# Optimization experiments

Hardware: AMD Instinct MI355X
Metric: run time of the kernel (lower is better)

Reference implementation:

```python
import jax, jax.numpy as jnp
import numpy as np

DIM = 1024
NUM_HEADS = 16
HEAD_DIM = DIM // NUM_HEADS
SCALE = HEAD_DIM ** (-0.5)


def setup_inputs() -> dict:
    key = jax.random.key(0)
    ks = jax.random.split(key, 10)
    b, nq, nkv = 1, 4096, 4096
    s = DIM ** -0.5
    return {
        "q": jax.random.normal(ks[0], (b, nq, DIM), jnp.float32),
        "kv": jax.random.normal(ks[1], (b, nkv, DIM), jnp.float32),
        "q_w": jax.random.normal(ks[2], (DIM, DIM), jnp.float32) * s,
        "q_b": jnp.zeros((DIM,), jnp.float32),
        "k_w": jax.random.normal(ks[3], (DIM, DIM), jnp.float32) * s,
        "k_b": jnp.zeros((DIM,), jnp.float32),
        "v_w": jax.random.normal(ks[4], (DIM, DIM), jnp.float32) * s,
        "v_b": jnp.zeros((DIM,), jnp.float32),
        "o_w": jax.random.normal(ks[5], (DIM, DIM), jnp.float32) * s,
        "o_b": jnp.zeros((DIM,), jnp.float32),
    }


def reference(q, kv, q_w, q_b, k_w, k_b, v_w, v_b, o_w, o_b):
    b, nq, _ = q.shape
    nkv = kv.shape[1]
    h, c = NUM_HEADS, HEAD_DIM
    # projections (torch Linear: x @ W^T + b); split into heads
    qh = (q @ q_w.T + q_b).reshape(b, nq, h, c).transpose(0, 2, 1, 3)   # b h nq c
    kh = (kv @ k_w.T + k_b).reshape(b, nkv, h, c).transpose(0, 2, 1, 3)  # b h nkv c
    vh = (kv @ v_w.T + v_b).reshape(b, nkv, h, c).transpose(0, 2, 1, 3)  # b h nkv c
    # full attention score matrix (non-fused, as in source)
    attn = jnp.einsum('bhqc,bhkc->bhqk', qh, kh) * SCALE
    attn = jax.nn.softmax(attn, axis=-1)
    out = jnp.einsum('bhqk,bhkc->bhqc', attn, vh)  # b h nq c
    out = out.transpose(0, 2, 1, 3).reshape(b, nq, h * c)
    out = out @ o_w.T + o_b
    return out
```

## Files before the change

kernel.cpp:

```cpp
#include <hip/hip_runtime.h>


typedef unsigned short ushort_t;
typedef unsigned short ushort4v __attribute__((ext_vector_type(4)));
typedef unsigned short ushort8 __attribute__((ext_vector_type(8)));
typedef __bf16 bf16x8 __attribute__((ext_vector_type(8)));
typedef float f32x4 __attribute__((ext_vector_type(4)));
typedef float f32x16 __attribute__((ext_vector_type(16)));
typedef unsigned int uint4v __attribute__((ext_vector_type(4)));

#define SEQ 4096
#define DIM 1024
#define NH 16
#define HD 64
#define QSCALE 0.18033688011112042f

__device__ inline ushort_t fcvt(float f) {
    return __builtin_bit_cast(ushort_t, (__bf16)f);
}
__device__ inline bf16x8 frag_of(ushort8 t) {
    return __builtin_bit_cast(bf16x8, t);
}
__device__ inline bf16x8 lds_frag(const ushort_t* p) {
    return frag_of(*(const ushort8*)p);
}
__device__ inline unsigned pk2(float a, float b) {
    return (unsigned)fcvt(a) | ((unsigned)fcvt(b) << 16);
}
__device__ inline void plswap(unsigned& a, unsigned& b) {
    asm("v_permlane32_swap_b32 %0, %1" : "+v"(a), "+v"(b));
}
__device__ inline int swz(int row, int col) {
    return row * 64 + (col ^ ((row & 7) << 3));
}
__device__ inline int xcd_swz(int bid, int nwg) {
    return (bid & 7) * (nwg >> 3) + (bid >> 3);
}
__device__ __attribute__((always_inline)) inline void gload16(
    const ushort_t* g, ushort_t* l)
{
    __builtin_amdgcn_global_load_lds(
        (const __attribute__((address_space(1))) void*)g,
        (__attribute__((address_space(3))) void*)l, 16, 0, 0);
}

__global__ __launch_bounds__(256) void cvt2(
    const float* __restrict__ s0, ushort_t* __restrict__ d0,
    const float* __restrict__ s1, ushort_t* __restrict__ d1, int n8)
{
    const float* s = blockIdx.y ? s1 : s0;
    ushort_t*    d = blockIdx.y ? d1 : d0;
    int i = blockIdx.x * 256 + threadIdx.x;
    if (i >= n8) return;
    const f32x4* sp = (const f32x4*)s + (size_t)i * 2;
    f32x4 a = sp[0], b = sp[1];
    ushort8 o;
    for (int k = 0; k < 4; ++k) { o[k] = fcvt(a[k]); o[k + 4] = fcvt(b[k]); }
    *((ushort8*)d + i) = o;
}

__global__ __launch_bounds__(256) void cvt4(
    const float* __restrict__ s0, ushort_t* __restrict__ d0,
    const float* __restrict__ s1, ushort_t* __restrict__ d1,
    const float* __restrict__ s2, ushort_t* __restrict__ d2,
    const float* __restrict__ s3, ushort_t* __restrict__ d3, int n8)
{
    const float* ss[4] = {s0, s1, s2, s3};
    ushort_t*    dd[4] = {d0, d1, d2, d3};
    const float* s = ss[blockIdx.y];
    ushort_t*    d = dd[blockIdx.y];
    int i = blockIdx.x * 256 + threadIdx.x;
    if (i >= n8) return;
    const f32x4* sp = (const f32x4*)s + (size_t)i * 2;
    f32x4 a = sp[0], b = sp[1];
    ushort8 o;
    for (int k = 0; k < 4; ++k) { o[k] = fcvt(a[k]); o[k + 4] = fcvt(b[k]); }
    *((ushort8*)d + i) = o;
}

template<int BM, int BN>
__device__ __attribute__((always_inline)) inline void gemm_core3(
    const ushort_t* __restrict__ A, const ushort_t* __restrict__ W,
    int m0, int n0, int tid, f32x4 (&acc)[BM / 32][BN / 32], ushort_t* sLDS)
{
    constexpr int TA = BM * 32;
    constexpr int TB = BN * 32;
    ushort_t* const aB0 = sLDS;
    ushort_t* const aB1 = sLDS + TA;
    ushort_t* const bB0 = sLDS + 2 * TA;
    ushort_t* const bB1 = sLDS + 2 * TA + TB;

    const int w    = tid >> 6;
    const int lane = tid & 63;
    const int quad = lane >> 4;
    const int l15  = lane & 15;
    const int wm   = w >> 1;
    const int wn   = w & 1;

    const int srow = lane >> 2;
    const int sch  = (((lane & 3) ^ ((lane >> 3) & 3)) << 3);
    const ushort_t* Ag = A + (size_t)(m0 + w * (BM / 4) + srow) * DIM + sch;
    const ushort_t* Bg = W + (size_t)(n0 + w * (BN / 4) + srow) * DIM + sch;
    const int aOff = w * (BM / 4) * 32;
    const int bOff = w * (BN / 4) * 32;

    for (int i = 0; i < BM / 64; ++i)
        gload16(Ag + (size_t)(i * 16) * DIM, aB0 + aOff + i * 512);
    for (int i = 0; i < BN / 64; ++i)
        gload16(Bg + (size_t)(i * 16) * DIM, bB0 + bOff + i * 512);
    __syncthreads();

    const int slot = (quad ^ ((l15 >> 1) & 3)) << 3;
    for (int it = 0; it < DIM / 32; ++it) {
        const int cur = it & 1;
        ushort_t* aC = cur ? aB1 : aB0;
        ushort_t* bC = cur ? bB1 : bB0;
        ushort_t* aN = cur ? aB0 : aB1;
        ushort_t* bN = cur ? bB0 : bB1;

        if (it + 1 < DIM / 32) {
            const int k0 = (it + 1) * 32;
            for (int i = 0; i < BM / 64; ++i)
                gload16(Ag + k0 + (size_t)(i * 16) * DIM, aN + aOff + i * 512);
            for (int i = 0; i < BN / 64; ++i)
                gload16(Bg + k0 + (size_t)(i * 16) * DIM, bN + bOff + i * 512);
        }

        bf16x8 af[BM / 32], bf[BN / 32];
        for (int i = 0; i < BM / 32; ++i) {
            int row = wm * (BM / 2) + i * 16 + l15;
            af[i] = lds_frag(aC + row * 32 + slot);
        }
        for (int j = 0; j < BN / 32; ++j) {
            int row = wn * (BN / 2) + j * 16 + l15;
            bf[j] = lds_frag(bC + row * 32 + slot);
        }
        for (int i = 0; i < BM / 32; ++i)
            for (int j = 0; j < BN / 32; ++j)
                acc[i][j] = __builtin_amdgcn_mfma_f32_16x16x32_bf16(
                    af[i], bf[j], acc[i][j], 0, 0, 0);
        __syncthreads();
    }
}

__global__ __launch_bounds__(256, 3) void proj3(
    const ushort_t* __restrict__ Qb, const ushort_t* __restrict__ KVb,
    const ushort_t* __restrict__ qwb, const ushort_t* __restrict__ kwb,
    const ushort_t* __restrict__ vwb,
    const float* __restrict__ q_b, const float* __restrict__ k_b,
    const float* __restrict__ v_b,
    ushort_t* __restrict__ Qp, ushort_t* __restrict__ Kp,
    ushort_t* __restrict__ VpT)
{
    __shared__ __align__(1024) ushort_t sLDS[17536];

    const int lb = xcd_swz(blockIdx.x, 768);
    const int z  = lb >> 8;
    const int r  = lb & 255;
    const int m0 = (r >> 3) * 128;
    const int n0 = (r & 7) * 128;

    const ushort_t* A = z ? KVb : Qb;
    const ushort_t* W = (z == 0) ? qwb : (z == 1 ? kwb : vwb);
    const float* bias = (z == 0) ? q_b : (z == 1 ? k_b : v_b);
    const int tid = threadIdx.x;

    f32x4 acc[4][4] = {};
    gemm_core3<128, 128>(A, W, m0, n0, tid, acc, sLDS);

    const int lane = tid & 63, quad = lane >> 4, l15 = lane & 15;
    const int wm = (tid >> 6) >> 1, wn = (tid >> 6) & 1;

    if (z == 2) {
        const int TSTR = 136;
        for (int j = 0; j < 4; ++j) {
            int col = wn * 64 + j * 16 + l15;
            float bj = bias[n0 + col];
            for (int i = 0; i < 4; ++i) {
                int row = wm * 64 + i * 16 + quad * 4;
                ushort4v o4;
                for (int r2 = 0; r2 < 4; ++r2) o4[r2] = fcvt(acc[i][j][r2] + bj);
                *(ushort4v*)(sLDS + col * TSTR + row) = o4;
            }
        }
        __syncthreads();
        const int vrow = tid >> 1;
        const int vc   = (tid & 1) * 64;
        ushort_t* dst = VpT + (size_t)(n0 + vrow) * SEQ + m0 + vc;
        const ushort_t* src = sLDS + vrow * TSTR + vc;
        for (int k = 0; k < 8; ++k)
            *(ushort8*)(dst + k * 8) = *(const ushort8*)(src + k * 8);
    } else {
        const float scale = (z == 0) ? QSCALE : 1.0f;
        ushort_t* C = z ? Kp : Qp;
        for (int j = 0; j < 4; ++j) {
            int col = n0 + wn * 64 + j * 16 + l15;
            float bj = bias[col];
            for (int i = 0; i < 4; ++i) {
                int row = m0 + wm * 64 + i * 16 + quad * 4;
                for (int r2 = 0; r2 < 4; ++r2)
                    C[(size_t)(row + r2) * DIM + col] =
                        fcvt((acc[i][j][r2] + bj) * scale);
            }
        }
    }
}

__global__ __launch_bounds__(256, 4) void gemm_out(
    const ushort_t* __restrict__ A, const ushort_t* __restrict__ W,
    const float* __restrict__ bias, float* __restrict__ C)
{
    __shared__ __align__(1024) ushort_t sLDS[8192];

    const int lb = xcd_swz(blockIdx.x, 1024);
    const int m0 = (lb >> 4) * 64;
    const int n0 = (lb & 15) * 64;
    const int tid = threadIdx.x;

    f32x4 acc[2][2] = {};
    gemm_core3<64, 64>(A, W, m0, n0, tid, acc, sLDS);

    const int lane = tid & 63, quad = lane >> 4, l15 = lane & 15;
    const int wm = (tid >> 6) >> 1, wn = (tid >> 6) & 1;
    for (int j = 0; j < 2; ++j) {
        int col = n0 + wn * 32 + j * 16 + l15;
        float bj = bias[col];
        for (int i = 0; i < 2; ++i) {
            int row = m0 + wm * 32 + i * 16 + quad * 4;
            for (int r = 0; r < 4; ++r)
                C[(size_t)(row + r) * DIM + col] = acc[i][j][r] + bj;
        }
    }
}

#define TILE 4096
#define BUFE (2 * TILE)
__global__ __launch_bounds__(256, 2) void attn_kernel(
    const ushort_t* __restrict__ Q, const ushort_t* __restrict__ K,
    const ushort_t* __restrict__ VT, ushort_t* __restrict__ O)
{
    __shared__ __align__(16) ushort_t sB[2 * BUFE];

    const int lb   = xcd_swz(blockIdx.x, 512);
    const int h    = lb >> 5;
    const int qblk = lb & 31;

    const int tid  = threadIdx.x;
    const int w    = tid >> 6;
    const int lane = tid & 63;
    const int l31  = lane & 31;
    const int hi   = lane >> 5;
    const int q0   = qblk * 128 + w * 32;
    const int hHD  = h * HD;

    const int srow0 = tid >> 3;
    const int srow1 = srow0 + 32;
    const int sch   = (tid & 7) << 3;
    const ushort_t* Kg0 = K  + (size_t)srow0 * DIM + hHD + sch;
    const ushort_t* Kg1 = K  + (size_t)srow1 * DIM + hHD + sch;
    const ushort_t* Vg0 = VT + (size_t)(hHD + srow0) * SEQ + sch;
    const ushort_t* Vg1 = VT + (size_t)(hHD + srow1) * SEQ + sch;
    const int lk0 = swz(srow0, sch), lk1 = swz(srow1, sch);

    const ushort_t* qb = Q + (size_t)(q0 + l31) * DIM + hHD + hi * 8;
    bf16x8 qf[4];
    for (int ks = 0; ks < 4; ++ks)
        qf[ks] = frag_of(*(const ushort8*)(qb + ks * 16));

    *(ushort8*)(sB + lk0)        = *(const ushort8*)(Kg0);
    *(ushort8*)(sB + lk1)        = *(const ushort8*)(Kg1);
    *(ushort8*)(sB + TILE + lk0) = *(const ushort8*)(Vg0);
    *(ushort8*)(sB + TILE + lk1) = *(const ushort8*)(Vg1);
    __syncthreads();

    f32x16 oacc[2] = {};
    float l_i = 0.f;

    for (int it = 0; it < SEQ / 64; ++it) {
        const int cur = it & 1;
        const int kvn = (it + 1) * 64;
        ushort_t* bK = sB + cur * BUFE;
        ushort_t* bV = bK + TILE;

        ushort8 gk0, gk1, gv0, gv1;
        if (kvn < SEQ) {
            gk0 = *(const ushort8*)(Kg0 + (size_t)kvn * DIM);
            gk1 = *(const ushort8*)(Kg1 + (size_t)kvn * DIM);
            gv0 = *(const ushort8*)(Vg0 + kvn);
            gv1 = *(const ushort8*)(Vg1 + kvn);
        }

        bf16x8 kf[8], vf[8];
        for (int t = 0; t < 2; ++t)
            for (int ks = 0; ks < 4; ++ks) {
                int r = t * 32 + l31;
                kf[t * 4 + ks] = lds_frag(bK + swz(r, ks * 16 + hi * 8));
            }
        for (int dt = 0; dt < 2; ++dt)
            for (int ks = 0; ks < 4; ++ks) {
                int r = dt * 32 + l31;
                vf[ks * 2 + dt] = lds_frag(bV + swz(r, ks * 16 + hi * 8));
            }

        f32x16 sacc[2] = {};
        for (int t = 0; t < 2; ++t)
            for (int ks = 0; ks < 4; ++ks)
                sacc[t] = __builtin_amdgcn_mfma_f32_32x32x16_bf16(
                    kf[t * 4 + ks], qf[ks], sacc[t], 0, 0, 0);

        float lp = 0.f;
        for (int t = 0; t < 2; ++t)
            for (int r = 0; r < 16; ++r) {
                float p = __builtin_amdgcn_exp2f(sacc[t][r]);
                sacc[t][r] = p;
                lp += p;
            }
        l_i += lp + __shfl_xor(lp, 32);

        for (int ks = 0; ks < 4; ++ks) {
            const int t = ks >> 1, s8 = (ks & 1) * 8;
            unsigned p00 = pk2(sacc[t][s8 + 0], sacc[t][s8 + 1]);
            unsigned p01 = pk2(sacc[t][s8 + 2], sacc[t][s8 + 3]);
            unsigned p10 = pk2(sacc[t][s8 + 4], sacc[t][s8 + 5]);
            unsigned p11 = pk2(sacc[t][s8 + 6], sacc[t][s8 + 7]);
            plswap(p00, p10);
            plswap(p01, p11);
            uint4v wv; wv[0] = p00; wv[1] = p01; wv[2] = p10; wv[3] = p11;
            bf16x8 pf = __builtin_bit_cast(bf16x8, wv);
            for (int dt = 0; dt < 2; ++dt)
                oacc[dt] = __builtin_amdgcn_mfma_f32_32x32x16_bf16(
                    vf[ks * 2 + dt], pf, oacc[dt], 0, 0, 0);
        }

        if (kvn < SEQ) {
            ushort_t* nB = sB + (cur ^ 1) * BUFE;
            *(ushort8*)(nB + lk0)        = gk0;
            *(ushort8*)(nB + lk1)        = gk1;
            *(ushort8*)(nB + TILE + lk0) = gv0;
            *(ushort8*)(nB + TILE + lk1) = gv1;
        }
        __syncthreads();
    }

    float inv = 1.f / l_i;
    int qrow = q0 + l31;
    for (int dt = 0; dt < 2; ++dt)
        for (int g = 0; g < 4; ++g) {
            ushort4v o4;
            for (int r = 0; r < 4; ++r) o4[r] = fcvt(oacc[dt][g * 4 + r] * inv);
            *(ushort4v*)(O + (size_t)qrow * DIM + hHD + dt * 32 + g * 8 + hi * 4) = o4;
        }
}

extern "C" void kernel_launch(void* const* d_in, const int* in_sizes, int n_in,
                              void* d_out, int out_size, void* d_ws, size_t ws_size,
                              hipStream_t stream)
{
    const float* q   = (const float*)d_in[0];
    const float* kv  = (const float*)d_in[1];
    const float* q_w = (const float*)d_in[2];
    const float* q_b = (const float*)d_in[3];
    const float* k_w = (const float*)d_in[4];
    const float* k_b = (const float*)d_in[5];
    const float* v_w = (const float*)d_in[6];
    const float* v_b = (const float*)d_in[7];
    const float* o_w = (const float*)d_in[8];
    const float* o_b = (const float*)d_in[9];
    float* out = (float*)d_out;

    const size_t SD = (size_t)SEQ * DIM;
    const size_t WW = (size_t)DIM * DIM;
    ushort_t* Qp  = (ushort_t*)d_ws;
    ushort_t* Kp  = Qp + SD;
    ushort_t* VpT = Kp + SD;
    ushort_t* AO  = VpT + SD;
    ushort_t* Qb  = AO;
    ushort_t* KVb = AO + SD;
    ushort_t* qwb = KVb + SD;
    ushort_t* kwb = qwb + WW;
    ushort_t* vwb = kwb + WW;
    ushort_t* owb = vwb + WW;

    cvt2<<<dim3((unsigned)(SD / 8 / 256), 2), 256, 0, stream>>>(
        q, Qb, kv, KVb, (int)(SD / 8));
    cvt4<<<dim3((unsigned)(WW / 8 / 256), 4), 256, 0, stream>>>(
        q_w, qwb, k_w, kwb, v_w, vwb, o_w, owb, (int)(WW / 8));

    proj3<<<dim3(768), 256, 0, stream>>>(
        Qb, KVb, qwb, kwb, vwb, q_b, k_b, v_b, Qp, Kp, VpT);
    attn_kernel<<<dim3(512), 256, 0, stream>>>(Qp, Kp, VpT, AO);
    gemm_out<<<dim3(1024), 256, 0, stream>>>(AO, owb, o_b, out);
}
```

Baseline: 245.7 us.

## Software-pipeline attention loop to overlap PV MFMA with next tile's softmax

```diff
diff --git a/kernel.cpp b/kernel.cpp
--- a/kernel.cpp
+++ b/kernel.cpp
@@ -275,31 +275,25 @@
 
     f32x16 oacc[2] = {};
     float l_i = 0.f;
-
-    for (int it = 0; it < SEQ / 64; ++it) {
-        const int cur = it & 1;
-        const int kvn = (it + 1) * 64;
-        ushort_t* bK = sB + cur * BUFE;
-        ushort_t* bV = bK + TILE;
-
-        ushort8 gk0, gk1, gv0, gv1;
-        if (kvn < SEQ) {
-            gk0 = *(const ushort8*)(Kg0 + (size_t)kvn * DIM);
-            gk1 = *(const ushort8*)(Kg1 + (size_t)kvn * DIM);
-            gv0 = *(const ushort8*)(Vg0 + kvn);
-            gv1 = *(const ushort8*)(Vg1 + kvn);
-        }
-
-        bf16x8 kf[8], vf[8];
+    uint4v pf_p[4];
+    bf16x8 vf_p[8];
+
+    {
+        ushort8 gk0 = *(const ushort8*)(Kg0 + (size_t)64 * DIM);
+        ushort8 gk1 = *(const ushort8*)(Kg1 + (size_t)64 * DIM);
+        ushort8 gv0 = *(const ushort8*)(Vg0 + 64);
+        ushort8 gv1 = *(const ushort8*)(Vg1 + 64);
+
+        bf16x8 kf[8];
         for (int t = 0; t < 2; ++t)
             for (int ks = 0; ks < 4; ++ks) {
                 int r = t * 32 + l31;
-                kf[t * 4 + ks] = lds_frag(bK + swz(r, ks * 16 + hi * 8));
+                kf[t * 4 + ks] = lds_frag(sB + swz(r, ks * 16 + hi * 8));
             }
         for (int dt = 0; dt < 2; ++dt)
             for (int ks = 0; ks < 4; ++ks) {
                 int r = dt * 32 + l31;
-                vf[ks * 2 + dt] = lds_frag(bV + swz(r, ks * 16 + hi * 8));
+                vf_p[ks * 2 + dt] = lds_frag(sB + TILE + swz(r, ks * 16 + hi * 8));
             }
 
         f32x16 sacc[2] = {};
@@ -326,10 +320,76 @@
             plswap(p00, p10);
             plswap(p01, p11);
             uint4v wv; wv[0] = p00; wv[1] = p01; wv[2] = p10; wv[3] = p11;
-            bf16x8 pf = __builtin_bit_cast(bf16x8, wv);
+            pf_p[ks] = wv;
+        }
+
+        ushort_t* nB = sB + BUFE;
+        *(ushort8*)(nB + lk0)        = gk0;
+        *(ushort8*)(nB + lk1)        = gk1;
+        *(ushort8*)(nB + TILE + lk0) = gv0;
+        *(ushort8*)(nB + TILE + lk1) = gv1;
+        __syncthreads();
+    }
+
+    for (int it = 1; it < SEQ / 64; ++it) {
+        const int cur = it & 1;
+        const int kvn = (it + 1) * 64;
+        ushort_t* bK = sB + cur * BUFE;
+        ushort_t* bV = bK + TILE;
+
+        ushort8 gk0, gk1, gv0, gv1;
+        if (kvn < SEQ) {
+            gk0 = *(const ushort8*)(Kg0 + (size_t)kvn * DIM);
+            gk1 = *(const ushort8*)(Kg1 + (size_t)kvn * DIM);
+            gv0 = *(const ushort8*)(Vg0 + kvn);
+            gv1 = *(const ushort8*)(Vg1 + kvn);
+        }
+
+        bf16x8 kf[8];
+        for (int t = 0; t < 2; ++t)
+            for (int ks = 0; ks < 4; ++ks) {
+                int r = t * 32 + l31;
+                kf[t * 4 + ks] = lds_frag(bK + swz(r, ks * 16 + hi * 8));
+            }
+
+        f32x16 sacc[2] = {};
+        for (int t = 0; t < 2; ++t)
+            for (int ks = 0; ks < 4; ++ks)
+                sacc[t] = __builtin_amdgcn_mfma_f32_32x32x16_bf16(
+                    kf[t * 4 + ks], qf[ks], sacc[t], 0, 0, 0);
+
+        for (int ks = 0; ks < 4; ++ks) {
+            bf16x8 pf = __builtin_bit_cast(bf16x8, pf_p[ks]);
             for (int dt = 0; dt < 2; ++dt)
                 oacc[dt] = __builtin_amdgcn_mfma_f32_32x32x16_bf16(
-                    vf[ks * 2 + dt], pf, oacc[dt], 0, 0, 0);
+                    vf_p[ks * 2 + dt], pf, oacc[dt], 0, 0, 0);
+        }
+
+        for (int dt = 0; dt < 2; ++dt)
+            for (int ks = 0; ks < 4; ++ks) {
+                int r = dt * 32 + l31;
+                vf_p[ks * 2 + dt] = lds_frag(bV + swz(r, ks * 16 + hi * 8));
+            }
+
+        float lp = 0.f;
+        for (int t = 0; t < 2; ++t)
+            for (int r = 0; r < 16; ++r) {
+                float p = __builtin_amdgcn_exp2f(sacc[t][r]);
+                sacc[t][r] = p;
+                lp += p;
+            }
+        l_i += lp + __shfl_xor(lp, 32);
+
+        for (int ks = 0; ks < 4; ++ks) {
+            const int t = ks >> 1, s8 = (ks & 1) * 8;
+            unsigned p00 = pk2(sacc[t][s8 + 0], sacc[t][s8 + 1]);
+            unsigned p01 = pk2(sacc[t][s8 + 2], sacc[t][s8 + 3]);
+            unsigned p10 = pk2(sacc[t][s8 + 4], sacc[t][s8 + 5]);
+            unsigned p11 = pk2(sacc[t][s8 + 6], sacc[t][s8 + 7]);
+            plswap(p00, p10);
+            plswap(p01, p11);
+            uint4v wv; wv[0] = p00; wv[1] = p01; wv[2] = p10; wv[3] = p11;
+            pf_p[ks] = wv;
         }
 
         if (kvn < SEQ) {
@@ -340,6 +400,13 @@
             *(ushort8*)(nB + TILE + lk1) = gv1;
         }
         __syncthreads();
+    }
+
+    for (int ks = 0; ks < 4; ++ks) {
+        bf16x8 pf = __builtin_bit_cast(bf16x8, pf_p[ks]);
+        for (int dt = 0; dt < 2; ++dt)
+            oacc[dt] = __builtin_amdgcn_mfma_f32_32x32x16_bf16(
+                vf_p[ks * 2 + dt], pf, oacc[dt], 0, 0, 0);
     }
 
     float inv = 1.f / l_i;
```

Result: no change. 242.2 us (-1.4%).

## Triple-buffer GEMM LDS staging with vmcnt-based waits instead of full syncs

Applied to the files above, without the earlier changes.

```diff
diff --git a/kernel.cpp b/kernel.cpp
--- a/kernel.cpp
+++ b/kernel.cpp
@@ -79,16 +79,15 @@
 }
 
 template<int BM, int BN>
-__device__ __attribute__((always_inline)) inline void gemm_core3(
+__device__ __attribute__((always_inline)) inline void gemm_core4(
     const ushort_t* __restrict__ A, const ushort_t* __restrict__ W,
     int m0, int n0, int tid, f32x4 (&acc)[BM / 32][BN / 32], ushort_t* sLDS)
 {
-    constexpr int TA = BM * 32;
-    constexpr int TB = BN * 32;
-    ushort_t* const aB0 = sLDS;
-    ushort_t* const aB1 = sLDS + TA;
-    ushort_t* const bB0 = sLDS + 2 * TA;
-    ushort_t* const bB1 = sLDS + 2 * TA + TB;
+    constexpr int TA  = BM * 32;
+    constexpr int TB  = BN * 32;
+    constexpr int TT  = TA + TB;
+    constexpr int LPW = BM / 64 + BN / 64;
+    constexpr int NST = DIM / 32;
 
     const int w    = tid >> 6;
     const int lane = tid & 63;
@@ -104,43 +103,54 @@
     const int aOff = w * (BM / 4) * 32;
     const int bOff = w * (BN / 4) * 32;
 
-    for (int i = 0; i < BM / 64; ++i)
-        gload16(Ag + (size_t)(i * 16) * DIM, aB0 + aOff + i * 512);
-    for (int i = 0; i < BN / 64; ++i)
-        gload16(Bg + (size_t)(i * 16) * DIM, bB0 + bOff + i * 512);
-    __syncthreads();
+    ushort_t* b0 = sLDS;
+    ushort_t* b1 = sLDS + TT;
+    ushort_t* b2 = sLDS + 2 * TT;
+
+#define STAGE4(buf, k0)                                                     \
+    do {                                                                    \
+        for (int i = 0; i < BM / 64; ++i)                                   \
+            gload16(Ag + (k0) + (size_t)(i * 16) * DIM,                     \
+                    (buf) + aOff + i * 512);                                \
+        for (int i = 0; i < BN / 64; ++i)                                   \
+            gload16(Bg + (k0) + (size_t)(i * 16) * DIM,                     \
+                    (buf) + TA + bOff + i * 512);                           \
+    } while (0)
+
+    STAGE4(b0, 0);
+    STAGE4(b1, 32);
 
     const int slot = (quad ^ ((l15 >> 1) & 3)) << 3;
-    for (int it = 0; it < DIM / 32; ++it) {
-        const int cur = it & 1;
-        ushort_t* aC = cur ? aB1 : aB0;
-        ushort_t* bC = cur ? bB1 : bB0;
-        ushort_t* aN = cur ? aB0 : aB1;
-        ushort_t* bN = cur ? bB0 : bB1;
-
-        if (it + 1 < DIM / 32) {
-            const int k0 = (it + 1) * 32;
-            for (int i = 0; i < BM / 64; ++i)
-                gload16(Ag + k0 + (size_t)(i * 16) * DIM, aN + aOff + i * 512);
-            for (int i = 0; i < BN / 64; ++i)
-                gload16(Bg + k0 + (size_t)(i * 16) * DIM, bN + bOff + i * 512);
-        }
+    for (int it = 0; it < NST; ++it) {
+        if (it < NST - 1)
+            asm volatile("s_waitcnt vmcnt(%0)" :: "i"(LPW) : "memory");
+        else
+            asm volatile("s_waitcnt vmcnt(0)" ::: "memory");
+        asm volatile("s_barrier" ::: "memory");
+
+        if (it + 2 < NST)
+            STAGE4(b2, (it + 2) * 32);
 
         bf16x8 af[BM / 32], bf[BN / 32];
         for (int i = 0; i < BM / 32; ++i) {
             int row = wm * (BM / 2) + i * 16 + l15;
-            af[i] = lds_frag(aC + row * 32 + slot);
+            af[i] = lds_frag(b0 + row * 32 + slot);
         }
         for (int j = 0; j < BN / 32; ++j) {
             int row = wn * (BN / 2) + j * 16 + l15;
-            bf[j] = lds_frag(bC + row * 32 + slot);
+            bf[j] = lds_frag(b0 + TA + row * 32 + slot);
         }
         for (int i = 0; i < BM / 32; ++i)
             for (int j = 0; j < BN / 32; ++j)
                 acc[i][j] = __builtin_amdgcn_mfma_f32_16x16x32_bf16(
                     af[i], bf[j], acc[i][j], 0, 0, 0);
-        __syncthreads();
+
+        asm volatile("s_waitcnt lgkmcnt(0)" ::: "memory");
+
+        ushort_t* t = b0; b0 = b1; b1 = b2; b2 = t;
     }
+#undef STAGE4
+    __syncthreads();
 }
 
 __global__ __launch_bounds__(256, 3) void proj3(
@@ -152,7 +162,7 @@
     ushort_t* __restrict__ Qp, ushort_t* __restrict__ Kp,
     ushort_t* __restrict__ VpT)
 {
-    __shared__ __align__(1024) ushort_t sLDS[17536];
+    __shared__ __align__(1024) ushort_t sLDS[24576];
 
     const int lb = xcd_swz(blockIdx.x, 768);
     const int z  = lb >> 8;
@@ -166,7 +176,7 @@
     const int tid = threadIdx.x;
 
     f32x4 acc[4][4] = {};
-    gemm_core3<128, 128>(A, W, m0, n0, tid, acc, sLDS);
+    gemm_core4<128, 128>(A, W, m0, n0, tid, acc, sLDS);
 
     const int lane = tid & 63, quad = lane >> 4, l15 = lane & 15;
     const int wm = (tid >> 6) >> 1, wn = (tid >> 6) & 1;
@@ -210,7 +220,7 @@
     const ushort_t* __restrict__ A, const ushort_t* __restrict__ W,
     const float* __restrict__ bias, float* __restrict__ C)
 {
-    __shared__ __align__(1024) ushort_t sLDS[8192];
+    __shared__ __align__(1024) ushort_t sLDS[12288];
 
     const int lb = xcd_swz(blockIdx.x, 1024);
     const int m0 = (lb >> 4) * 64;
@@ -218,7 +228,7 @@
     const int tid = threadIdx.x;
 
     f32x4 acc[2][2] = {};
-    gemm_core3<64, 64>(A, W, m0, n0, tid, acc, sLDS);
+    gemm_core4<64, 64>(A, W, m0, n0, tid, acc, sLDS);
 
     const int lane = tid & 63, quad = lane >> 4, l15 = lane & 15;
     const int wm = (tid >> 6) >> 1, wn = (tid >> 6) & 1;
```

Result: no change. 246.0 us (+0.1%).
